# Kernel tuning notes

Hardware: AMD Instinct MI355X
Metric: run time of the kernel (lower is better)

Reference implementation:

```python
import jax, jax.numpy as jnp
import numpy as np

N = 500_000     # nodes
E = 8_000_000   # edges
F_IN = 16       # input node features
H = 10          # hidden_size (from args)
G = 1024        # graphs in batch
L = 3           # num_layers (from args)
BN_EPS = 1e-5


def setup_inputs() -> dict:
    key = jax.random.key(0)
    ks = jax.random.split(key, 16)
    s = 0.3  # keep activations tame through ReLU MLPs
    return {
        "x": jax.random.normal(ks[0], (N, F_IN), dtype=jnp.float32),
        "edge_index": jax.random.randint(ks[1], (2, E), 0, N, dtype=jnp.int32),
        "batch": jnp.sort(jax.random.randint(ks[2], (N,), 0, G, dtype=jnp.int32)),
        "preW": s * jax.random.normal(ks[3], (F_IN, H), dtype=jnp.float32),
        "preb": s * jax.random.normal(ks[4], (H,), dtype=jnp.float32),
        "convW1": s * jax.random.normal(ks[5], (L, H, H), dtype=jnp.float32),
        "convb1": s * jax.random.normal(ks[6], (L, H), dtype=jnp.float32),
        "convW2": s * jax.random.normal(ks[7], (L, H, H), dtype=jnp.float32),
        "convb2": s * jax.random.normal(ks[8], (L, H), dtype=jnp.float32),
        "bn_gamma": jnp.ones((L - 1, H), dtype=jnp.float32),
        "bn_beta": jnp.zeros((L - 1, H), dtype=jnp.float32),
        "postW1": s * jax.random.normal(ks[9], (H, H), dtype=jnp.float32),
        "postb1": s * jax.random.normal(ks[10], (H,), dtype=jnp.float32),
        "postW2": s * jax.random.normal(ks[11], (H, 1), dtype=jnp.float32),
        "postb2": s * jax.random.normal(ks[12], (1,), dtype=jnp.float32),
    }


def reference(x, edge_index, batch, preW, preb, convW1, convb1, convW2, convb2,
              bn_gamma, bn_beta, postW1, postb1, postW2, postb2):
    src, dst = edge_index[0], edge_index[1]

    def gin_conv(h, l):
        # GINConv (eps=0): MLP(h + sum_{j in N(i)} h_j), scatter-add over edges
        agg = jnp.zeros_like(h).at[dst].add(h[src])
        z = h + agg
        z = jnp.maximum(z @ convW1[l] + convb1[l], 0.0)
        return z @ convW2[l] + convb2[l]

    def batchnorm(h, l):
        # training-mode BatchNorm1d: batch stats, biased variance
        mean = jnp.mean(h, axis=0)
        var = jnp.mean((h - mean) ** 2, axis=0)
        return (h - mean) * jax.lax.rsqrt(var + BN_EPS) * bn_gamma[l] + bn_beta[l]

    h = x @ preW + preb                      # pre_mp: [N, H]
    for l in range(L - 1):                   # convs[:-1] followed by bn
        h = batchnorm(gin_conv(h, l), l)
    h = gin_conv(h, L - 1)                   # last conv, no bn

    # global_mean_pool over graph ids
    sums = jax.ops.segment_sum(h, batch, num_segments=G)          # [G, H]
    counts = jax.ops.segment_sum(jnp.ones((h.shape[0],), h.dtype), batch,
                                 num_segments=G)                   # [G]
    pooled = sums / jnp.maximum(counts, 1.0)[:, None]

    out = jnp.maximum(pooled @ postW1 + postb1, 0.0) @ postW2 + postb2  # [G, 1]
    return out
```

## Files before the change

kernel.cpp:

```cpp
#include <hip/hip_runtime.h>
#include <hip/hip_fp16.h>


static constexpr int HF = 10;
static constexpr int HPH = 16;
static constexpr int FIN = 16;
static constexpr int BLK = 256;
static constexpr int UB = 8;
static constexpr int SREP = 128;
static constexpr int BWB = 13;
static constexpr int SRB = 19;
static constexpr int EPB = 4096;

static inline size_t alignup(size_t x) { return (x + 255) & ~(size_t)255; }

__device__ inline void unpack_add(uint4 a, uint a2, float* z) {
    float2 t;
    t = __half22float2(*reinterpret_cast<const __half2*>(&a.x)); z[0] += t.x; z[1] += t.y;
    t = __half22float2(*reinterpret_cast<const __half2*>(&a.y)); z[2] += t.x; z[3] += t.y;
    t = __half22float2(*reinterpret_cast<const __half2*>(&a.z)); z[4] += t.x; z[5] += t.y;
    t = __half22float2(*reinterpret_cast<const __half2*>(&a.w)); z[6] += t.x; z[7] += t.y;
    t = __half22float2(*reinterpret_cast<const __half2*>(&a2));  z[8] += t.x; z[9] += t.y;
}

__device__ inline void unpack_fma(uint4 a, uint a2, float w, float* z) {
    float2 t;
    t = __half22float2(*reinterpret_cast<const __half2*>(&a.x)); z[0] = fmaf(w, t.x, z[0]); z[1] = fmaf(w, t.y, z[1]);
    t = __half22float2(*reinterpret_cast<const __half2*>(&a.y)); z[2] = fmaf(w, t.x, z[2]); z[3] = fmaf(w, t.y, z[3]);
    t = __half22float2(*reinterpret_cast<const __half2*>(&a.z)); z[4] = fmaf(w, t.x, z[4]); z[5] = fmaf(w, t.y, z[5]);
    t = __half22float2(*reinterpret_cast<const __half2*>(&a.w)); z[6] = fmaf(w, t.x, z[6]); z[7] = fmaf(w, t.y, z[7]);
    t = __half22float2(*reinterpret_cast<const __half2*>(&a2));  z[8] = fmaf(w, t.x, z[8]); z[9] = fmaf(w, t.y, z[9]);
}

__device__ inline void store_row_f16(__half* row, const float* o) {
    __half2 p01 = __floats2half2_rn(o[0], o[1]);
    __half2 p23 = __floats2half2_rn(o[2], o[3]);
    __half2 p45 = __floats2half2_rn(o[4], o[5]);
    __half2 p67 = __floats2half2_rn(o[6], o[7]);
    __half2 p89 = __floats2half2_rn(o[8], o[9]);
    uint4 w;
    w.x = *reinterpret_cast<uint*>(&p01);
    w.y = *reinterpret_cast<uint*>(&p23);
    w.z = *reinterpret_cast<uint*>(&p45);
    w.w = *reinterpret_cast<uint*>(&p67);
    *reinterpret_cast<uint4*>(row) = w;
    *reinterpret_cast<uint*>(row + 8) = *reinterpret_cast<uint*>(&p89);
}

__device__ inline void stats_block_reduce(const float* o, float* stats) {
    __shared__ float sred[BLK / 64][32];
#pragma unroll
    for (int j = 0; j < HF; ++j) {
        float s = o[j];
        float q = o[j] * o[j];
#pragma unroll
        for (int off = 32; off > 0; off >>= 1) {
            s += __shfl_down(s, off);
            q += __shfl_down(q, off);
        }
        if ((threadIdx.x & 63) == 0) {
            sred[threadIdx.x >> 6][j] = s;
            sred[threadIdx.x >> 6][16 + j] = q;
        }
    }
    __syncthreads();
    int t = threadIdx.x;
    if (t < 32) {
        bool lo = (t < HF);
        bool hi = (t >= 16 && t < 16 + HF);
        if (lo || hi) {
            float v = sred[0][t] + sred[1][t] + sred[2][t] + sred[3][t];
            unsafeAtomicAdd(&stats[(blockIdx.x & (SREP - 1)) * 32 + t], v);
        }
    }
}

__global__ void pre_mp_f16_kernel(const float* __restrict__ x, const float* __restrict__ W,
                                  const float* __restrict__ b, __half* __restrict__ h, int N) {
    int i = blockIdx.x * blockDim.x + threadIdx.x;
    if (i >= N) return;
    const float4* xr = (const float4*)(x + (size_t)i * FIN);
    float xv[FIN];
    float4 x0 = xr[0], x1 = xr[1], x2 = xr[2], x3 = xr[3];
    xv[0]=x0.x; xv[1]=x0.y; xv[2]=x0.z; xv[3]=x0.w;
    xv[4]=x1.x; xv[5]=x1.y; xv[6]=x1.z; xv[7]=x1.w;
    xv[8]=x2.x; xv[9]=x2.y; xv[10]=x2.z; xv[11]=x2.w;
    xv[12]=x3.x; xv[13]=x3.y; xv[14]=x3.z; xv[15]=x3.w;
    float acc[HF];
#pragma unroll
    for (int j = 0; j < HF; ++j) acc[j] = b[j];
#pragma unroll
    for (int k = 0; k < FIN; ++k) {
#pragma unroll
        for (int j = 0; j < HF; ++j) acc[j] = fmaf(xv[k], W[k * HF + j], acc[j]);
    }
    store_row_f16(h + (size_t)i * HPH, acc);
}

__global__ void pre_mp_kernel(const float* __restrict__ x, const float* __restrict__ W,
                              const float* __restrict__ b, float* __restrict__ h, int N) {
    int i = blockIdx.x * blockDim.x + threadIdx.x;
    if (i >= N) return;
    const float4* xr = (const float4*)(x + (size_t)i * FIN);
    float xv[FIN];
    float4 x0 = xr[0], x1 = xr[1], x2 = xr[2], x3 = xr[3];
    xv[0]=x0.x; xv[1]=x0.y; xv[2]=x0.z; xv[3]=x0.w;
    xv[4]=x1.x; xv[5]=x1.y; xv[6]=x1.z; xv[7]=x1.w;
    xv[8]=x2.x; xv[9]=x2.y; xv[10]=x2.z; xv[11]=x2.w;
    xv[12]=x3.x; xv[13]=x3.y; xv[14]=x3.z; xv[15]=x3.w;
    float acc[HF];
#pragma unroll
    for (int j = 0; j < HF; ++j) acc[j] = b[j];
#pragma unroll
    for (int k = 0; k < FIN; ++k) {
#pragma unroll
        for (int j = 0; j < HF; ++j) acc[j] = fmaf(xv[k], W[k * HF + j], acc[j]);
    }
    float* hr = h + (size_t)i * HF;
#pragma unroll
    for (int j = 0; j < HF; ++j) hr[j] = acc[j];
}

__global__ void blocksum_kernel(const int* __restrict__ deg, int* __restrict__ bsum, int M) {
    int i = blockIdx.x * BLK + threadIdx.x;
    int v = (i < M) ? deg[i] : 0;
#pragma unroll
    for (int off = 32; off > 0; off >>= 1) v += __shfl_down(v, off);
    __shared__ int sm[BLK / 64];
    if ((threadIdx.x & 63) == 0) sm[threadIdx.x >> 6] = v;
    __syncthreads();
    if (threadIdx.x == 0) {
        int t = 0;
#pragma unroll
        for (int w = 0; w < BLK / 64; ++w) t += sm[w];
        bsum[blockIdx.x] = t;
    }
}

__global__ void scan_bsum_kernel(int* __restrict__ bs, int nb) {
    __shared__ int sm[1024];
    int running = 0;
    for (int base = 0; base < nb; base += 1024) {
        int i = base + (int)threadIdx.x;
        int v = (i < nb) ? bs[i] : 0;
        sm[threadIdx.x] = v;
        __syncthreads();
        for (int off = 1; off < 1024; off <<= 1) {
            int t = (threadIdx.x >= (unsigned)off) ? sm[threadIdx.x - off] : 0;
            __syncthreads();
            sm[threadIdx.x] += t;
            __syncthreads();
        }
        int incl = sm[threadIdx.x];
        if (i < nb) bs[i] = running + incl - v;
        int chunk_total = sm[1023];
        __syncthreads();
        running += chunk_total;
    }
}

__global__ void rowptr_kernel(const int* __restrict__ deg, const int* __restrict__ bsum,
                              int* __restrict__ rowptr, int* cursor, int M) {
    int i = blockIdx.x * BLK + threadIdx.x;
    int v = (i < M) ? deg[i] : 0;
    __shared__ int sm[BLK];
    sm[threadIdx.x] = v;
    __syncthreads();
    for (int off = 1; off < BLK; off <<= 1) {
        int t = (threadIdx.x >= (unsigned)off) ? sm[threadIdx.x - off] : 0;
        __syncthreads();
        sm[threadIdx.x] += t;
        __syncthreads();
    }
    int excl = sm[threadIdx.x] - v + bsum[blockIdx.x];
    if (i < M) {
        rowptr[i] = excl;
        cursor[i] = excl;
    }
}

__global__ void bucket_hist_kernel(const int* __restrict__ dst, int* __restrict__ bcount,
                                   int E, int B) {
    __shared__ int lcount[64];
    if (threadIdx.x < B) lcount[threadIdx.x] = 0;
    __syncthreads();
    int start = blockIdx.x * EPB;
    int end = min(start + EPB, E);
    for (int e = start + threadIdx.x; e < end; e += BLK)
        atomicAdd(&lcount[dst[e] >> BWB], 1);
    __syncthreads();
    if (threadIdx.x < B && lcount[threadIdx.x] > 0)
        atomicAdd(&bcount[threadIdx.x], lcount[threadIdx.x]);
}

__global__ void bucket_scan_kernel(const int* __restrict__ bcount, int* __restrict__ bbase,
                                   int* __restrict__ bcursor, int B) {
    if (threadIdx.x == 0) {
        int run = 0;
        for (int b = 0; b < B; ++b) {
            bbase[b] = run;
            bcursor[b] = run;
            run += bcount[b];
        }
        bbase[B] = run;
    }
}

__global__ void partition_kernel(const int* __restrict__ src, const int* __restrict__ dst,
                                 int* __restrict__ bcursor, uint* __restrict__ packed,
                                 int E, int B) {
    __shared__ int lcount[64], lbase[64], lcur[64];
    int start = blockIdx.x * EPB;
    int end = min(start + EPB, E);
    if (threadIdx.x < B) lcount[threadIdx.x] = 0;
    __syncthreads();
    for (int e = start + threadIdx.x; e < end; e += BLK)
        atomicAdd(&lcount[dst[e] >> BWB], 1);
    __syncthreads();
    if (threadIdx.x < B) {
        lbase[threadIdx.x] = (lcount[threadIdx.x] > 0)
                           ? atomicAdd(&bcursor[threadIdx.x], lcount[threadIdx.x]) : 0;
        lcur[threadIdx.x] = 0;
    }
    __syncthreads();
    for (int e = start + threadIdx.x; e < end; e += BLK) {
        int d = dst[e];
        int b = d >> BWB;
        int p = lbase[b] + atomicAdd(&lcur[b], 1);
        packed[p] = ((uint)(d & ((1 << BWB) - 1)) << SRB) | (uint)src[e];
    }
}

__device__ inline int find_bucket(const int* sbase, int B, int p) {
    int lo = 0, hi = B;
    while (hi - lo > 1) {
        int mid = (lo + hi) >> 1;
        if (p >= sbase[mid]) lo = mid; else hi = mid;
    }
    return lo;
}

__global__ void l2_hist_kernel(const uint* __restrict__ packed1, const int* __restrict__ bbase,
                               int* __restrict__ gcount, int E, int B) {
    __shared__ int sbase[65];
    __shared__ int lcount[128];
    __shared__ int g0s;
    if (threadIdx.x <= B) sbase[threadIdx.x] = bbase[threadIdx.x];
    if (threadIdx.x < 128) lcount[threadIdx.x] = 0;
    __syncthreads();
    int start = blockIdx.x * EPB;
    int end = min(start + EPB, E);
    if (start >= E) return;
    if (threadIdx.x == 0) g0s = find_bucket(sbase, B, start) << 6;
    __syncthreads();
    int g0 = g0s;
    for (int p = start + threadIdx.x; p < end; p += BLK) {
        uint v = packed1[p];
        int b = find_bucket(sbase, B, p);
        int g = (b << 6) | (((int)(v >> SRB)) >> 7);
        atomicAdd(&lcount[g - g0], 1);
    }
    __syncthreads();
    if (threadIdx.x < 128 && lcount[threadIdx.x] > 0)
        atomicAdd(&gcount[g0 + threadIdx.x], lcount[threadIdx.x]);
}

__global__ void l2_scan_kernel(const int* __restrict__ gcount, int* __restrict__ gbase,
                               int* __restrict__ gcursor, int NG) {
    __shared__ int sm[1024];
    int running = 0;
    for (int b0 = 0; b0 < NG; b0 += 1024) {
        int i = b0 + (int)threadIdx.x;
        int v = (i < NG) ? gcount[i] : 0;
        sm[threadIdx.x] = v;
        __syncthreads();
        for (int off = 1; off < 1024; off <<= 1) {
            int t = (threadIdx.x >= (unsigned)off) ? sm[threadIdx.x - off] : 0;
            __syncthreads();
            sm[threadIdx.x] += t;
            __syncthreads();
        }
        int incl = sm[threadIdx.x];
        if (i < NG) { gbase[i] = running + incl - v; gcursor[i] = running + incl - v; }
        int tot = sm[1023];
        __syncthreads();
        running += tot;
    }
    if (threadIdx.x == 0) gbase[NG] = running;
}

__global__ void l2_place_kernel(const uint* __restrict__ packed1, const int* __restrict__ bbase,
                                int* __restrict__ gcursor, uint* __restrict__ packed2,
                                int E, int B) {
    __shared__ int sbase[65];
    __shared__ int lcount[128], lbase[128], lcur[128];
    __shared__ int g0s;
    if (threadIdx.x <= B) sbase[threadIdx.x] = bbase[threadIdx.x];
    if (threadIdx.x < 128) lcount[threadIdx.x] = 0;
    __syncthreads();
    int start = blockIdx.x * EPB;
    int end = min(start + EPB, E);
    if (start >= E) return;
    if (threadIdx.x == 0) g0s = find_bucket(sbase, B, start) << 6;
    __syncthreads();
    int g0 = g0s;
    for (int p = start + threadIdx.x; p < end; p += BLK) {
        uint v = packed1[p];
        int b = find_bucket(sbase, B, p);
        int bin = ((b << 6) | (((int)(v >> SRB)) >> 7)) - g0;
        atomicAdd(&lcount[bin], 1);
    }
    __syncthreads();
    if (threadIdx.x < 128) {
        lbase[threadIdx.x] = (lcount[threadIdx.x] > 0)
                           ? atomicAdd(&gcursor[g0 + threadIdx.x], lcount[threadIdx.x]) : 0;
        lcur[threadIdx.x] = 0;
    }
    __syncthreads();
    for (int p = start + threadIdx.x; p < end; p += BLK) {
        uint v = packed1[p];
        int b = find_bucket(sbase, B, p);
        int bin = ((b << 6) | (((int)(v >> SRB)) >> 7)) - g0;
        packed2[lbase[bin] + atomicAdd(&lcur[bin], 1)] = v;
    }
}

__global__ void l3_sort_kernel(const uint* __restrict__ packed2, const int* __restrict__ gbase,
                               int* __restrict__ csr2, int* __restrict__ rowptr,
                               int N, int C, int cbits, int E) {
    __shared__ int cnt[1024];
    __shared__ int bas[1024];
    __shared__ int tsum[256];
    int g = blockIdx.x;
    int start = gbase[g], end = gbase[g + 1];
    int dstbase = g << 7;
    for (int t = threadIdx.x; t < 1024; t += BLK) cnt[t] = 0;
    __syncthreads();
    for (int p = start + (int)threadIdx.x; p < end; p += BLK) {
        uint v = packed2[p];
        int s = (int)(v & ((1u << SRB) - 1));
        int dl7 = ((int)(v >> SRB)) & 127;
        atomicAdd(&cnt[dl7 * C + (s >> cbits)], 1);
    }
    __syncthreads();
    int tid = threadIdx.x;
    int c0 = cnt[4 * tid], c1 = cnt[4 * tid + 1], c2 = cnt[4 * tid + 2], c3 = cnt[4 * tid + 3];
    int mysum = c0 + c1 + c2 + c3;
    tsum[tid] = mysum;
    __syncthreads();
    for (int off = 1; off < 256; off <<= 1) {
        int t2 = (tid >= off) ? tsum[tid - off] : 0;
        __syncthreads();
        tsum[tid] += t2;
        __syncthreads();
    }
    int excl = tsum[tid] - mysum;
    bas[4 * tid] = excl;
    bas[4 * tid + 1] = excl + c0;
    bas[4 * tid + 2] = excl + c0 + c1;
    bas[4 * tid + 3] = excl + c0 + c1 + c2;
    __syncthreads();
    for (int t = threadIdx.x; t < 128; t += BLK) {
        int dstn = dstbase + t;
        if (dstn < N) rowptr[dstn] = start + bas[t * C];
    }
    for (int t = threadIdx.x; t < 1024; t += BLK) cnt[t] = 0;
    __syncthreads();
    for (int p = start + (int)threadIdx.x; p < end; p += BLK) {
        uint v = packed2[p];
        int s = (int)(v & ((1u << SRB) - 1));
        int dl7 = ((int)(v >> SRB)) & 127;
        int key = dl7 * C + (s >> cbits);
        int pos = start + bas[key] + atomicAdd(&cnt[key], 1);
        csr2[pos] = s;
    }
}

__global__ void hist_kernel(const int* __restrict__ idx, int* __restrict__ deg, int E) {
    int e = blockIdx.x * blockDim.x + threadIdx.x;
    if (e >= E) return;
    atomicAdd(&deg[idx[e]], 1);
}

__global__ void fill_kernel(const int* __restrict__ src, const int* __restrict__ dst,
                            int* __restrict__ cursor, int* __restrict__ csr, int E) {
    int e = blockIdx.x * blockDim.x + threadIdx.x;
    if (e >= E) return;
    int pos = atomicAdd(&cursor[dst[e]], 1);
    csr[pos] = src[e];
}

template <bool BN, bool STATS, bool POOL>
__global__ void __launch_bounds__(BLK) conv_sorted_kernel(
        const __half* __restrict__ hin, const int* __restrict__ rowptr,
        const int* __restrict__ csr, const float* __restrict__ ss,
        const float* __restrict__ W1, const float* __restrict__ b1,
        const float* __restrict__ W2, const float* __restrict__ b2,
        __half* __restrict__ hout, int N, int E, float* stats,
        const int* __restrict__ batch, float* pool, float* cnt) {
    int i = blockIdx.x * blockDim.x + threadIdx.x;
    bool act = i < N;
    float o[HF];
    int g = 0x7fffffff;
    if (act) {
        float z[HF];
#pragma unroll
        for (int j = 0; j < HF; ++j) z[j] = 0.0f;
        {
            const __half* hp = hin + (size_t)i * HPH;
            uint4 r = *reinterpret_cast<const uint4*>(hp);
            uint r2 = *reinterpret_cast<const uint*>(hp + 8);
            unpack_add(r, r2, z);
        }
        int base = rowptr[i];
        int end = (i + 1 < N) ? rowptr[i + 1] : E;
        int d = end - base;
        for (int k0 = 0; k0 < d; k0 += UB) {
            int s[UB];
            float w[UB];
#pragma unroll
            for (int u = 0; u < UB; ++u) {
                int kk = k0 + u;
                int kc = kk < d ? kk : d - 1;
                s[u] = csr[base + kc];
                w[u] = kk < d ? 1.0f : 0.0f;
            }
            uint4 a[UB];
            uint a2[UB];
#pragma unroll
            for (int u = 0; u < UB; ++u) {
                const __half* sp = hin + (size_t)s[u] * HPH;
                a[u]  = *reinterpret_cast<const uint4*>(sp);
                a2[u] = *reinterpret_cast<const uint*>(sp + 8);
            }
#pragma unroll
            for (int u = 0; u < UB; ++u) unpack_fma(a[u], a2[u], w[u], z);
        }
        if (BN) {
            float dp1 = (float)(d + 1);
#pragma unroll
            for (int j = 0; j < HF; ++j) z[j] = fmaf(z[j], ss[j], dp1 * ss[HF + j]);
        }
        float t[HF];
#pragma unroll
        for (int j = 0; j < HF; ++j) {
            float a = b1[j];
#pragma unroll
            for (int k = 0; k < HF; ++k) a = fmaf(z[k], W1[k * HF + j], a);
            t[j] = fmaxf(a, 0.0f);
        }
#pragma unroll
        for (int j = 0; j < HF; ++j) {
            float a = b2[j];
#pragma unroll
            for (int k = 0; k < HF; ++k) a = fmaf(t[k], W2[k * HF + j], a);
            o[j] = a;
        }
        if (!POOL) {
            store_row_f16(hout + (size_t)i * HPH, o);
        } else {
            g = batch[i];
        }
    } else {
#pragma unroll
        for (int j = 0; j < HF; ++j) o[j] = 0.0f;
    }
    if (STATS) stats_block_reduce(o, stats);
    if (POOL) {
        int lane = threadIdx.x & 63;
        float c1 = act ? 1.0f : 0.0f;
#pragma unroll
        for (int off = 1; off < 64; off <<= 1) {
            int gu = __shfl_up(g, off);
            float cu = __shfl_up(c1, off);
            bool take = (lane >= off) && (gu == g);
            if (take) c1 += cu;
#pragma unroll
            for (int j = 0; j < HF; ++j) {
                float vu = __shfl_up(o[j], off);
                if (take) o[j] += vu;
            }
        }
        int gn = __shfl_down(g, 1);
        bool last = (lane == 63) || (gn != g);
        if (act && last) {
#pragma unroll
            for (int j = 0; j < HF; ++j) unsafeAtomicAdd(&pool[(size_t)g * HF + j], o[j]);
            unsafeAtomicAdd(&cnt[g], c1);
        }
    }
}

template <bool BN, bool STATS, bool POOL>
__global__ void __launch_bounds__(BLK) conv_kernel(
                            const __half* __restrict__ hin,
                            const int* __restrict__ rowptr, const int* __restrict__ deg,
                            const int* __restrict__ csr, const float* __restrict__ ss,
                            const float* __restrict__ W1, const float* __restrict__ b1,
                            const float* __restrict__ W2, const float* __restrict__ b2,
                            __half* __restrict__ hout, int N, float* stats,
                            const int* __restrict__ batch, float* pool, float* cnt) {
    int i = blockIdx.x * blockDim.x + threadIdx.x;
    bool act = i < N;
    float o[HF];
    int g = 0x7fffffff;
    if (act) {
        float z[HF];
#pragma unroll
        for (int j = 0; j < HF; ++j) z[j] = 0.0f;
        {
            const __half* hp = hin + (size_t)i * HPH;
            uint4 r = *reinterpret_cast<const uint4*>(hp);
            uint r2 = *reinterpret_cast<const uint*>(hp + 8);
            unpack_add(r, r2, z);
        }
        int base = rowptr[i];
        int d = deg[i];
        for (int k0 = 0; k0 < d; k0 += UB) {
            int s[UB];
            float w[UB];
#pragma unroll
            for (int u = 0; u < UB; ++u) {
                int kk = k0 + u;
                int kc = kk < d ? kk : d - 1;
                s[u] = csr[base + kc];
                w[u] = kk < d ? 1.0f : 0.0f;
            }
            uint4 a[UB];
            uint a2[UB];
#pragma unroll
            for (int u = 0; u < UB; ++u) {
                const __half* sp = hin + (size_t)s[u] * HPH;
                a[u]  = *reinterpret_cast<const uint4*>(sp);
                a2[u] = *reinterpret_cast<const uint*>(sp + 8);
            }
#pragma unroll
            for (int u = 0; u < UB; ++u) unpack_fma(a[u], a2[u], w[u], z);
        }
        if (BN) {
            float dp1 = (float)(d + 1);
#pragma unroll
            for (int j = 0; j < HF; ++j) z[j] = fmaf(z[j], ss[j], dp1 * ss[HF + j]);
        }
        float t[HF];
#pragma unroll
        for (int j = 0; j < HF; ++j) {
            float a = b1[j];
#pragma unroll
            for (int k = 0; k < HF; ++k) a = fmaf(z[k], W1[k * HF + j], a);
            t[j] = fmaxf(a, 0.0f);
        }
#pragma unroll
        for (int j = 0; j < HF; ++j) {
            float a = b2[j];
#pragma unroll
            for (int k = 0; k < HF; ++k) a = fmaf(t[k], W2[k * HF + j], a);
            o[j] = a;
        }
        if (!POOL) {
            store_row_f16(hout + (size_t)i * HPH, o);
        } else {
            g = batch[i];
        }
    } else {
#pragma unroll
        for (int j = 0; j < HF; ++j) o[j] = 0.0f;
    }
    if (STATS) stats_block_reduce(o, stats);
    if (POOL) {
        int lane = threadIdx.x & 63;
        float c1 = act ? 1.0f : 0.0f;
#pragma unroll
        for (int off = 1; off < 64; off <<= 1) {
            int gu = __shfl_up(g, off);
            float cu = __shfl_up(c1, off);
            bool take = (lane >= off) && (gu == g);
            if (take) c1 += cu;
#pragma unroll
            for (int j = 0; j < HF; ++j) {
                float vu = __shfl_up(o[j], off);
                if (take) o[j] += vu;
            }
        }
        int gn = __shfl_down(g, 1);
        bool last = (lane == 63) || (gn != g);
        if (act && last) {
#pragma unroll
            for (int j = 0; j < HF; ++j) unsafeAtomicAdd(&pool[(size_t)g * HF + j], o[j]);
            unsafeAtomicAdd(&cnt[g], c1);
        }
    }
}

__global__ void bn_finalize_kernel(const float* __restrict__ stats,
                                   const float* __restrict__ gamma,
                                   const float* __restrict__ beta,
                                   float* __restrict__ ss, float invN, int R) {
    int j = threadIdx.x;
    if (j >= HF) return;
    float sm = 0.0f, sq = 0.0f;
    for (int r = 0; r < R; ++r) {
        sm += stats[r * 32 + j];
        sq += stats[r * 32 + 16 + j];
    }
    float mean = sm * invN;
    float var = sq * invN - mean * mean;
    float sc = gamma[j] * rsqrtf(var + 1e-5f);
    ss[j] = sc;
    ss[HF + j] = beta[j] - mean * sc;
}

__global__ void head_kernel(const float* __restrict__ pool, const float* __restrict__ cnt,
                            const float* __restrict__ W1, const float* __restrict__ b1,
                            const float* __restrict__ W2, const float* __restrict__ b2,
                            float* __restrict__ out, int G) {
    int g = blockIdx.x * blockDim.x + threadIdx.x;
    if (g >= G) return;
    float inv = 1.0f / fmaxf(cnt[g], 1.0f);
    float p[HF];
    const float* pr = pool + (size_t)g * HF;
#pragma unroll
    for (int j = 0; j < HF; ++j) p[j] = pr[j] * inv;
    float acc = b2[0];
#pragma unroll
    for (int j = 0; j < HF; ++j) {
        float a = b1[j];
#pragma unroll
        for (int k = 0; k < HF; ++k) a = fmaf(p[k], W1[k * HF + j], a);
        acc = fmaf(fmaxf(a, 0.0f), W2[j], acc);
    }
    out[g] = acc;
}

template <bool BN>
__global__ void scatter_kernel(const int* __restrict__ src, const int* __restrict__ dst,
                               const float* __restrict__ h, const float* __restrict__ ss,
                               float* agg, int E) {
    int e = blockIdx.x * blockDim.x + threadIdx.x;
    if (e >= E) return;
    int s = src[e];
    int d = dst[e];
    const float* hr = h + (size_t)s * HF;
    float* ar = agg + (size_t)d * HF;
#pragma unroll
    for (int j = 0; j < HF; ++j) {
        float v = hr[j];
        if (BN) v = fmaf(v, ss[j], ss[HF + j]);
        unsafeAtomicAdd(&ar[j], v);
    }
}

template <bool BN, bool STATS>
__global__ void update_kernel(const float* __restrict__ h, const float* agg,
                              const float* __restrict__ ss,
                              const float* __restrict__ W1, const float* __restrict__ b1,
                              const float* __restrict__ W2, const float* __restrict__ b2,
                              float* out, int N, float* stats) {
    int i = blockIdx.x * blockDim.x + threadIdx.x;
    float o[HF];
    bool act = (i < N);
    if (act) {
        float z[HF];
        const float* hr = h + (size_t)i * HF;
        const float* ar = agg + (size_t)i * HF;
#pragma unroll
        for (int j = 0; j < HF; ++j) {
            float v = hr[j];
            if (BN) v = fmaf(v, ss[j], ss[HF + j]);
            z[j] = v + ar[j];
        }
        float t[HF];
#pragma unroll
        for (int j = 0; j < HF; ++j) {
            float a = b1[j];
#pragma unroll
            for (int k = 0; k < HF; ++k) a = fmaf(z[k], W1[k * HF + j], a);
            t[j] = fmaxf(a, 0.0f);
        }
        float* orow = out + (size_t)i * HF;
#pragma unroll
        for (int j = 0; j < HF; ++j) {
            float a = b2[j];
#pragma unroll
            for (int k = 0; k < HF; ++k) a = fmaf(t[k], W2[k * HF + j], a);
            o[j] = a;
            orow[j] = a;
        }
    } else {
#pragma unroll
        for (int j = 0; j < HF; ++j) o[j] = 0.0f;
    }
    if (STATS) {
#pragma unroll
        for (int j = 0; j < HF; ++j) {
            float s = o[j];
            float q = o[j] * o[j];
#pragma unroll
            for (int off = 32; off > 0; off >>= 1) {
                s += __shfl_down(s, off);
                q += __shfl_down(q, off);
            }
            if ((threadIdx.x & 63) == 0) {
                unsafeAtomicAdd(&stats[j], s);
                unsafeAtomicAdd(&stats[16 + j], q);
            }
        }
    }
}

__global__ void pool_atomic_kernel(const float* __restrict__ h, const int* __restrict__ batch,
                                   float* pool, float* cnt, int N) {
    int i = blockIdx.x * blockDim.x + threadIdx.x;
    if (i >= N) return;
    int g = batch[i];
    const float* hr = h + (size_t)i * HF;
    float* pr = pool + (size_t)g * HF;
#pragma unroll
    for (int j = 0; j < HF; ++j) unsafeAtomicAdd(&pr[j], hr[j]);
    unsafeAtomicAdd(&cnt[g], 1.0f);
}

extern "C" void kernel_launch(void* const* d_in, const int* in_sizes, int n_in,
                              void* d_out, int out_size, void* d_ws, size_t ws_size,
                              hipStream_t stream) {
    const float* x      = (const float*)d_in[0];
    const int*   ei     = (const int*)d_in[1];
    const int*   batch  = (const int*)d_in[2];
    const float* preW   = (const float*)d_in[3];
    const float* preb   = (const float*)d_in[4];
    const float* convW1 = (const float*)d_in[5];
    const float* convb1 = (const float*)d_in[6];
    const float* convW2 = (const float*)d_in[7];
    const float* convb2 = (const float*)d_in[8];
    const float* gamma  = (const float*)d_in[9];
    const float* beta   = (const float*)d_in[10];
    const float* postW1 = (const float*)d_in[11];
    const float* postb1 = (const float*)d_in[12];
    const float* postW2 = (const float*)d_in[13];
    const float* postb2 = (const float*)d_in[14];

    const int N = in_sizes[0] / FIN;
    const int E = in_sizes[1] / 2;
    const int G = out_size;
    const int* src = ei;
    const int* dst = ei + E;

    const int gN = (N + BLK - 1) / BLK;
    const int gE = (E + BLK - 1) / BLK;
    const int gG = (G + BLK - 1) / BLK;
    const int gP = (E + EPB - 1) / EPB;
    const float invN = 1.0f / (float)N;
    char* base = (char*)d_ws;

    const size_t statsFloats = (size_t)SREP * 32;
    const size_t smallFloats = 2 * statsFloats + 64 + 256 + (size_t)G * (HF + 1);

    const int cbits = 16;
    const int C = (N + (1 << cbits) - 1) >> cbits;
    const int B = (N + (1 << BWB) - 1) >> BWB;
    const int NG = B * 64;
    size_t ebytes = alignup((size_t)E * 4);

    size_t off1 = 0;
    auto take1 = [&](size_t bytes) { size_t o = off1; off1 += alignup(bytes); return o; };
    size_t pk1_o  = take1(ebytes);
    size_t pk2_o  = take1(ebytes);
    size_t h0_o1  = take1((size_t)N * HPH * 2);
    size_t h1_o1  = take1((size_t)N * HPH * 2);
    size_t rp_o   = take1((size_t)(N + 4) * 4);
    size_t gg_o   = take1((size_t)(3 * NG + 8) * 4);
    size_t sm_o1  = take1(smallFloats * 4);

    size_t off2 = 0;
    auto take2 = [&](size_t bytes) { size_t o = off2; off2 += alignup(bytes); return o; };
    size_t csr_o2 = take2((size_t)E * 4);
    size_t h0_o2  = take2((size_t)N * HPH * 2);
    size_t h1_o2  = take2((size_t)N * HPH * 2);
    size_t deg_o2 = take2((size_t)N * 4);
    size_t row_o2 = take2((size_t)N * 4);
    size_t cur_o2 = take2((size_t)N * 4);
    size_t bs_o2  = take2((size_t)gN * 4);
    size_t sm_o2  = take2(smallFloats * 4);

    bool tier1_ok = (off1 <= ws_size) && (C >= 2) && (C <= 8) && (B <= 64) &&
                    (N <= (1 << SRB));

    if (tier1_ok) {
        int*    csr2   = (int*)(base + pk1_o);
        uint*   packed1= (uint*)(base + pk1_o);
        uint*   packed2= (uint*)(base + pk2_o);
        __half* h0     = (__half*)(base + h0_o1);
        __half* h1     = (__half*)(base + h1_o1);
        int*    rowptr = (int*)(base + rp_o);
        int*    gcount = (int*)(base + gg_o);
        int*    gbase  = gcount + NG;
        int*    gcursor= gbase + NG + 4;
        float*  small  = (float*)(base + sm_o1);
        float* stats0 = small;
        float* stats1 = small + statsFloats;
        float* ss0    = small + 2 * statsFloats;
        float* ss1    = ss0 + 32;
        int*   bcount = (int*)(ss1 + 32);
        int*   bbase  = bcount + 64;
        int*   bcursor= bbase + 66;
        float* pool   = (float*)(bcursor + 64 + 2);
        float* cnt    = pool + (size_t)G * HF;

        pre_mp_f16_kernel<<<gN, BLK, 0, stream>>>(x, preW, preb, h0, N);

        hipMemsetAsync(stats0, 0, 2 * statsFloats * 4, stream);
        hipMemsetAsync(bcount, 0, 64 * 4, stream);
        hipMemsetAsync(gcount, 0, (size_t)NG * 4, stream);
        hipMemsetAsync(pool, 0, (size_t)G * (HF + 1) * 4, stream);

        bucket_hist_kernel<<<gP, BLK, 0, stream>>>(dst, bcount, E, B);
        bucket_scan_kernel<<<1, 64, 0, stream>>>(bcount, bbase, bcursor, B);
        partition_kernel<<<gP, BLK, 0, stream>>>(src, dst, bcursor, packed1, E, B);
        l2_hist_kernel<<<gP, BLK, 0, stream>>>(packed1, bbase, gcount, E, B);
        l2_scan_kernel<<<1, 1024, 0, stream>>>(gcount, gbase, gcursor, NG);
        l2_place_kernel<<<gP, BLK, 0, stream>>>(packed1, bbase, gcursor, packed2, E, B);
        l3_sort_kernel<<<NG, BLK, 0, stream>>>(packed2, gbase, csr2, rowptr, N, C, cbits, E);

        conv_sorted_kernel<false, true, false><<<gN, BLK, 0, stream>>>(h0, rowptr, csr2,
            nullptr, convW1 + 0 * HF * HF, convb1 + 0 * HF, convW2 + 0 * HF * HF,
            convb2 + 0 * HF, h1, N, E, stats0, nullptr, nullptr, nullptr);
        bn_finalize_kernel<<<1, 64, 0, stream>>>(stats0, gamma + 0 * HF, beta + 0 * HF, ss0, invN, SREP);

        conv_sorted_kernel<true, true, false><<<gN, BLK, 0, stream>>>(h1, rowptr, csr2,
            ss0, convW1 + 1 * HF * HF, convb1 + 1 * HF, convW2 + 1 * HF * HF,
            convb2 + 1 * HF, h0, N, E, stats1, nullptr, nullptr, nullptr);
        bn_finalize_kernel<<<1, 64, 0, stream>>>(stats1, gamma + 1 * HF, beta + 1 * HF, ss1, invN, SREP);

        conv_sorted_kernel<true, false, true><<<gN, BLK, 0, stream>>>(h0, rowptr, csr2,
            ss1, convW1 + 2 * HF * HF, convb1 + 2 * HF, convW2 + 2 * HF * HF,
            convb2 + 2 * HF, nullptr, N, E, nullptr, batch, pool, cnt);

        head_kernel<<<gG, BLK, 0, stream>>>(pool, cnt, postW1, postb1, postW2, postb2,
                                            (float*)d_out, G);
    } else if (off2 <= ws_size) {
        int*    csr    = (int*)(base + csr_o2);
        __half* h0     = (__half*)(base + h0_o2);
        __half* h1     = (__half*)(base + h1_o2);
        int*    deg    = (int*)(base + deg_o2);
        int*    rowptr = (int*)(base + row_o2);
        int*    cursor = (int*)(base + cur_o2);
        int*    bsum   = (int*)(base + bs_o2);
        float*  small  = (float*)(base + sm_o2);
        float* stats0 = small;
        float* stats1 = small + statsFloats;
        float* ss0    = small + 2 * statsFloats;
        float* ss1    = ss0 + 32;
        float* pool   = ss1 + 32 + 256;
        float* cnt    = pool + (size_t)G * HF;

        pre_mp_f16_kernel<<<gN, BLK, 0, stream>>>(x, preW, preb, h0, N);

        hipMemsetAsync(deg, 0, (size_t)N * 4, stream);
        hipMemsetAsync(stats0, 0, 2 * statsFloats * 4, stream);
        hipMemsetAsync(pool, 0, (size_t)G * (HF + 1) * 4, stream);
        hist_kernel<<<gE, BLK, 0, stream>>>(dst, deg, E);
        blocksum_kernel<<<gN, BLK, 0, stream>>>(deg, bsum, N);
        scan_bsum_kernel<<<1, 1024, 0, stream>>>(bsum, gN);
        rowptr_kernel<<<gN, BLK, 0, stream>>>(deg, bsum, rowptr, cursor, N);
        fill_kernel<<<gE, BLK, 0, stream>>>(src, dst, cursor, csr, E);

        conv_kernel<false, true, false><<<gN, BLK, 0, stream>>>(h0, rowptr, deg, csr, nullptr,
            convW1 + 0 * HF * HF, convb1 + 0 * HF, convW2 + 0 * HF * HF, convb2 + 0 * HF,
            h1, N, stats0, nullptr, nullptr, nullptr);
        bn_finalize_kernel<<<1, 64, 0, stream>>>(stats0, gamma + 0 * HF, beta + 0 * HF, ss0, invN, SREP);

        conv_kernel<true, true, false><<<gN, BLK, 0, stream>>>(h1, rowptr, deg, csr, ss0,
            convW1 + 1 * HF * HF, convb1 + 1 * HF, convW2 + 1 * HF * HF, convb2 + 1 * HF,
            h0, N, stats1, nullptr, nullptr, nullptr);
        bn_finalize_kernel<<<1, 64, 0, stream>>>(stats1, gamma + 1 * HF, beta + 1 * HF, ss1, invN, SREP);

        conv_kernel<true, false, true><<<gN, BLK, 0, stream>>>(h0, rowptr, deg, csr, ss1,
            convW1 + 2 * HF * HF, convb1 + 2 * HF, convW2 + 2 * HF * HF, convb2 + 2 * HF,
            nullptr, N, nullptr, batch, pool, cnt);

        head_kernel<<<gG, BLK, 0, stream>>>(pool, cnt, postW1, postb1, postW2, postb2,
                                            (float*)d_out, G);
    } else {
        size_t nh = (size_t)N * HF * sizeof(float);
        float* buf0 = (float*)base;
        float* buf1 = (float*)(base + nh);
        float* small = (float*)(base + 2 * nh);
        float* stats = small;
        float* ss0   = small + 32;
        float* ss1   = small + 64;
        float* pool  = small + 96;
        float* cnt   = pool + (size_t)G * HF;

        pre_mp_kernel<<<gN, BLK, 0, stream>>>(x, preW, preb, buf0, N);

        hipMemsetAsync(buf1, 0, nh, stream);
        hipMemsetAsync(stats, 0, 32 * 4, stream);
        scatter_kernel<false><<<gE, BLK, 0, stream>>>(src, dst, buf0, nullptr, buf1, E);
        update_kernel<false, true><<<gN, BLK, 0, stream>>>(buf0, buf1, nullptr,
            convW1 + 0 * HF * HF, convb1 + 0 * HF, convW2 + 0 * HF * HF, convb2 + 0 * HF,
            buf1, N, stats);
        bn_finalize_kernel<<<1, 64, 0, stream>>>(stats, gamma + 0 * HF, beta + 0 * HF, ss0, invN, 1);

        hipMemsetAsync(buf0, 0, nh, stream);
        hipMemsetAsync(stats, 0, 32 * 4, stream);
        scatter_kernel<true><<<gE, BLK, 0, stream>>>(src, dst, buf1, ss0, buf0, E);
        update_kernel<true, true><<<gN, BLK, 0, stream>>>(buf1, buf0, ss0,
            convW1 + 1 * HF * HF, convb1 + 1 * HF, convW2 + 1 * HF * HF, convb2 + 1 * HF,
            buf0, N, stats);
        bn_finalize_kernel<<<1, 64, 0, stream>>>(stats, gamma + 1 * HF, beta + 1 * HF, ss1, invN, 1);

        hipMemsetAsync(buf1, 0, nh, stream);
        scatter_kernel<true><<<gE, BLK, 0, stream>>>(src, dst, buf0, ss1, buf1, E);
        update_kernel<true, false><<<gN, BLK, 0, stream>>>(buf0, buf1, ss1,
            convW1 + 2 * HF * HF, convb1 + 2 * HF, convW2 + 2 * HF * HF, convb2 + 2 * HF,
            buf1, N, nullptr);

        hipMemsetAsync(pool, 0, (size_t)G * (HF + 1) * sizeof(float), stream);
        pool_atomic_kernel<<<gN, BLK, 0, stream>>>(buf1, batch, pool, cnt, N);
        head_kernel<<<gG, BLK, 0, stream>>>(pool, cnt, postW1, postb1, postW2, postb2,
                                            (float*)d_out, G);
    }
}
```

Measured before the change: 693.2 us.

## Replace per-node rowptr with per-source-chunk row pointers in GIN conv

The sort kernel now stores a row pointer for every (destination node, source chunk) pair instead of one per node, and the conv kernel walks the C source-chunk segments in order. Inside each chunk, neighbours are gathered two at a time rather than with the 8-wide masked unrolled loop. The likely aim is to drop the padded dummy loads of the masked loop and keep all threads of a block reading rows from the same source-chunk region at roughly the same time, improving cache locality. In exchange it adds N*C row-pointer storage and reads, and exposes less memory-level parallelism per thread than the 8-wide batch did.

```diff
diff --git a/kernel.cpp b/kernel.cpp
--- a/kernel.cpp
+++ b/kernel.cpp
@@ -326,7 +326,7 @@
 }
 
 __global__ void l3_sort_kernel(const uint* __restrict__ packed2, const int* __restrict__ gbase,
-                               int* __restrict__ csr2, int* __restrict__ rowptr,
+                               int* __restrict__ csr2, int* __restrict__ rowptr2,
                                int N, int C, int cbits, int E) {
     __shared__ int cnt[1024];
     __shared__ int bas[1024];
@@ -334,6 +334,7 @@
     int g = blockIdx.x;
     int start = gbase[g], end = gbase[g + 1];
     int dstbase = g << 7;
+    int nb = 128 * C;
     for (int t = threadIdx.x; t < 1024; t += BLK) cnt[t] = 0;
     __syncthreads();
     for (int p = start + (int)threadIdx.x; p < end; p += BLK) {
@@ -360,9 +361,10 @@
     bas[4 * tid + 2] = excl + c0 + c1;
     bas[4 * tid + 3] = excl + c0 + c1 + c2;
     __syncthreads();
-    for (int t = threadIdx.x; t < 128; t += BLK) {
-        int dstn = dstbase + t;
-        if (dstn < N) rowptr[dstn] = start + bas[t * C];
+    size_t slotbase = (size_t)g * nb;
+    for (int t = threadIdx.x; t < nb; t += BLK) {
+        int dstn = dstbase + t / C;
+        if (dstn < N) rowptr2[slotbase + t] = start + bas[t];
     }
     for (int t = threadIdx.x; t < 1024; t += BLK) cnt[t] = 0;
     __syncthreads();
@@ -391,12 +393,12 @@
 }
 
 template <bool BN, bool STATS, bool POOL>
-__global__ void __launch_bounds__(BLK) conv_sorted_kernel(
-        const __half* __restrict__ hin, const int* __restrict__ rowptr,
+__global__ void __launch_bounds__(BLK) conv_chunked_kernel(
+        const __half* __restrict__ hin, const int* __restrict__ rp2,
         const int* __restrict__ csr, const float* __restrict__ ss,
         const float* __restrict__ W1, const float* __restrict__ b1,
         const float* __restrict__ W2, const float* __restrict__ b2,
-        __half* __restrict__ hout, int N, int E, float* stats,
+        __half* __restrict__ hout, int N, int C, int E, float* stats,
         const int* __restrict__ batch, float* pool, float* cnt) {
     int i = blockIdx.x * blockDim.x + threadIdx.x;
     bool act = i < N;
@@ -412,30 +414,35 @@
             uint r2 = *reinterpret_cast<const uint*>(hp + 8);
             unpack_add(r, r2, z);
         }
-        int base = rowptr[i];
-        int end = (i + 1 < N) ? rowptr[i + 1] : E;
-        int d = end - base;
-        for (int k0 = 0; k0 < d; k0 += UB) {
-            int s[UB];
-            float w[UB];
-#pragma unroll
-            for (int u = 0; u < UB; ++u) {
-                int kk = k0 + u;
-                int kc = kk < d ? kk : d - 1;
-                s[u] = csr[base + kc];
-                w[u] = kk < d ? 1.0f : 0.0f;
+        size_t m0 = (size_t)i * C;
+        size_t mend = (size_t)N * C;
+        int b = rp2[m0];
+        int row0 = b;
+        for (int c = 0; c < C; ++c) {
+            size_t mn = m0 + c + 1;
+            int e2 = (mn < mend) ? rp2[mn] : E;
+            int k = b;
+            for (; k + 2 <= e2; k += 2) {
+                int s0 = csr[k], s1 = csr[k + 1];
+                const __half* p0 = hin + (size_t)s0 * HPH;
+                const __half* p1 = hin + (size_t)s1 * HPH;
+                uint4 a0 = *reinterpret_cast<const uint4*>(p0);
+                uint  b0 = *reinterpret_cast<const uint*>(p0 + 8);
+                uint4 a1 = *reinterpret_cast<const uint4*>(p1);
+                uint  b1v = *reinterpret_cast<const uint*>(p1 + 8);
+                unpack_add(a0, b0, z);
+                unpack_add(a1, b1v, z);
             }
-            uint4 a[UB];
-            uint a2[UB];
-#pragma unroll
-            for (int u = 0; u < UB; ++u) {
-                const __half* sp = hin + (size_t)s[u] * HPH;
-                a[u]  = *reinterpret_cast<const uint4*>(sp);
-                a2[u] = *reinterpret_cast<const uint*>(sp + 8);
+            if (k < e2) {
+                int s0 = csr[k];
+                const __half* p0 = hin + (size_t)s0 * HPH;
+                uint4 a0 = *reinterpret_cast<const uint4*>(p0);
+                uint  b0 = *reinterpret_cast<const uint*>(p0 + 8);
+                unpack_add(a0, b0, z);
             }
-#pragma unroll
-            for (int u = 0; u < UB; ++u) unpack_fma(a[u], a2[u], w[u], z);
-        }
+            b = e2;
+        }
+        int d = b - row0;
         if (BN) {
             float dp1 = (float)(d + 1);
 #pragma unroll
@@ -446,14 +453,14 @@
         for (int j = 0; j < HF; ++j) {
             float a = b1[j];
 #pragma unroll
-            for (int k = 0; k < HF; ++k) a = fmaf(z[k], W1[k * HF + j], a);
+            for (int k2 = 0; k2 < HF; ++k2) a = fmaf(z[k2], W1[k2 * HF + j], a);
             t[j] = fmaxf(a, 0.0f);
         }
 #pragma unroll
         for (int j = 0; j < HF; ++j) {
             float a = b2[j];
 #pragma unroll
-            for (int k = 0; k < HF; ++k) a = fmaf(t[k], W2[k * HF + j], a);
+            for (int k2 = 0; k2 < HF; ++k2) a = fmaf(t[k2], W2[k2 * HF + j], a);
             o[j] = a;
         }
         if (!POOL) {
@@ -759,6 +766,7 @@
     const int C = (N + (1 << cbits) - 1) >> cbits;
     const int B = (N + (1 << BWB) - 1) >> BWB;
     const int NG = B * 64;
+    const size_t M = (size_t)N * C;
     size_t ebytes = alignup((size_t)E * 4);
 
     size_t off1 = 0;
@@ -767,7 +775,7 @@
     size_t pk2_o  = take1(ebytes);
     size_t h0_o1  = take1((size_t)N * HPH * 2);
     size_t h1_o1  = take1((size_t)N * HPH * 2);
-    size_t rp_o   = take1((size_t)(N + 4) * 4);
+    size_t rp2_o  = take1((M + 8) * 4);
     size_t gg_o   = take1((size_t)(3 * NG + 8) * 4);
     size_t sm_o1  = take1(smallFloats * 4);
 
@@ -791,7 +799,7 @@
         uint*   packed2= (uint*)(base + pk2_o);
         __half* h0     = (__half*)(base + h0_o1);
         __half* h1     = (__half*)(base + h1_o1);
-        int*    rowptr = (int*)(base + rp_o);
+        int*    rp2    = (int*)(base + rp2_o);
         int*    gcount = (int*)(base + gg_o);
         int*    gbase  = gcount + NG;
         int*    gcursor= gbase + NG + 4;
@@ -819,21 +827,21 @@
         l2_hist_kernel<<<gP, BLK, 0, stream>>>(packed1, bbase, gcount, E, B);
         l2_scan_kernel<<<1, 1024, 0, stream>>>(gcount, gbase, gcursor, NG);
         l2_place_kernel<<<gP, BLK, 0, stream>>>(packed1, bbase, gcursor, packed2, E, B);
-        l3_sort_kernel<<<NG, BLK, 0, stream>>>(packed2, gbase, csr2, rowptr, N, C, cbits, E);
-
-        conv_sorted_kernel<false, true, false><<<gN, BLK, 0, stream>>>(h0, rowptr, csr2,
+        l3_sort_kernel<<<NG, BLK, 0, stream>>>(packed2, gbase, csr2, rp2, N, C, cbits, E);
+
+        conv_chunked_kernel<false, true, false><<<gN, BLK, 0, stream>>>(h0, rp2, csr2,
             nullptr, convW1 + 0 * HF * HF, convb1 + 0 * HF, convW2 + 0 * HF * HF,
-            convb2 + 0 * HF, h1, N, E, stats0, nullptr, nullptr, nullptr);
+            convb2 + 0 * HF, h1, N, C, E, stats0, nullptr, nullptr, nullptr);
         bn_finalize_kernel<<<1, 64, 0, stream>>>(stats0, gamma + 0 * HF, beta + 0 * HF, ss0, invN, SREP);
 
-        conv_sorted_kernel<true, true, false><<<gN, BLK, 0, stream>>>(h1, rowptr, csr2,
+        conv_chunked_kernel<true, true, false><<<gN, BLK, 0, stream>>>(h1, rp2, csr2,
             ss0, convW1 + 1 * HF * HF, convb1 + 1 * HF, convW2 + 1 * HF * HF,
-            convb2 + 1 * HF, h0, N, E, stats1, nullptr, nullptr, nullptr);
+            convb2 + 1 * HF, h0, N, C, E, stats1, nullptr, nullptr, nullptr);
         bn_finalize_kernel<<<1, 64, 0, stream>>>(stats1, gamma + 1 * HF, beta + 1 * HF, ss1, invN, SREP);
 
-        conv_sorted_kernel<true, false, true><<<gN, BLK, 0, stream>>>(h0, rowptr, csr2,
+        conv_chunked_kernel<true, false, true><<<gN, BLK, 0, stream>>>(h0, rp2, csr2,
             ss1, convW1 + 2 * HF * HF, convb1 + 2 * HF, convW2 + 2 * HF * HF,
-            convb2 + 2 * HF, nullptr, N, E, nullptr, batch, pool, cnt);
+            convb2 + 2 * HF, nullptr, N, C, E, nullptr, batch, pool, cnt);
 
         head_kernel<<<gG, BLK, 0, stream>>>(pool, cnt, postW1, postb1, postW2, postb2,
                                             (float*)d_out, G);
```

Result: slower. 813.7 us (+17.4%).
